# Performance work log

Hardware: AMD Instinct MI355X
Metric: run time of the kernel (lower is better)

## Reference

```python
import jax, jax.numpy as jnp
import numpy as np

N = 50000      # nodes
F_IN = 500     # in_channels
MID = 64       # mid_layer_channel
H = 2          # heads
OUT = 40       # out_channels
E = 800000     # edges per order
ORDER = 3
NEG_SLOPE = 0.2


def _gat(x, edge_index, W, a_src, a_dst, b, concat):
    # PyG-style GATConv (eval mode, dropout off), with self loops.
    n = x.shape[0]
    heads, ch = a_src.shape
    h = (x @ W).reshape(n, heads, ch)                    # [N,H,C]
    loop = jnp.arange(n)
    src = jnp.concatenate([edge_index[0], loop])
    dst = jnp.concatenate([edge_index[1], loop])
    al_s = jnp.sum(h * a_src, axis=-1)                   # [N,H]
    al_d = jnp.sum(h * a_dst, axis=-1)                   # [N,H]
    e = jax.nn.leaky_relu(al_s[src] + al_d[dst], NEG_SLOPE)   # [Etot,H]
    m = jax.ops.segment_max(e, dst, num_segments=n)      # softmax over incoming edges per dst
    ex = jnp.exp(e - m[dst])
    den = jax.ops.segment_sum(ex, dst, num_segments=n)
    alpha = ex / (den[dst] + 1e-16)
    out = jax.ops.segment_sum(alpha[:, :, None] * h[src], dst, num_segments=n)  # [N,H,C]
    if concat:
        return out.reshape(n, heads * ch) + b
    return out.mean(axis=1) + b


def _aggr(states, Wmix, wfin):
    # NOrderAggrConv (depth=2): mix order states with [order,order] weights + ELU,
    # then reduce to a single state with a learned [order] combination.
    h = jnp.stack(states, axis=1)                        # [N,order,C]
    h = jax.nn.elu(jnp.einsum('nkc,kj->njc', h, Wmix))
    return jnp.einsum('nkc,k->nc', h, wfin)


def setup_inputs():
    key = jax.random.key(0)
    ks = jax.random.split(key, 40)
    d = {}
    d['node_feature'] = jax.random.normal(ks[0], (N, F_IN), jnp.float32)
    for o in range(ORDER):
        d[f'adj{o}'] = jax.random.randint(ks[1 + o], (2, E), 0, N)
    i = 4
    s = 0.05
    layer_dims = [(F_IN, MID, H * MID), (MID * H, OUT, OUT)]
    for l, (fin, c, bdim) in enumerate(layer_dims):
        for o in range(ORDER):
            d[f'W_{l}_{o}'] = jax.random.normal(ks[i], (fin, H * c), jnp.float32) * s; i += 1
            d[f'as_{l}_{o}'] = jax.random.normal(ks[i], (H, c), jnp.float32) * s; i += 1
            d[f'ad_{l}_{o}'] = jax.random.normal(ks[i], (H, c), jnp.float32) * s; i += 1
            d[f'b_{l}_{o}'] = jnp.zeros((bdim,), jnp.float32)
    for l in range(2):
        d[f'agg{l}_W'] = jax.random.normal(ks[i], (ORDER, ORDER), jnp.float32) * 0.5; i += 1
        d[f'agg{l}_w'] = jnp.full((ORDER,), 1.0 / ORDER, jnp.float32)
    return d


def reference(node_feature, adj0, adj1, adj2,
              W_0_0, as_0_0, ad_0_0, b_0_0,
              W_0_1, as_0_1, ad_0_1, b_0_1,
              W_0_2, as_0_2, ad_0_2, b_0_2,
              W_1_0, as_1_0, ad_1_0, b_1_0,
              W_1_1, as_1_1, ad_1_1, b_1_1,
              W_1_2, as_1_2, ad_1_2, b_1_2,
              agg0_W, agg0_w, agg1_W, agg1_w):
    adjs = (adj0, adj1, adj2)
    p0 = ((W_0_0, as_0_0, ad_0_0, b_0_0),
          (W_0_1, as_0_1, ad_0_1, b_0_1),
          (W_0_2, as_0_2, ad_0_2, b_0_2))
    p1 = ((W_1_0, as_1_0, ad_1_0, b_1_0),
          (W_1_1, as_1_1, ad_1_1, b_1_1),
          (W_1_2, as_1_2, ad_1_2, b_1_2))
    aggs = ((agg0_W, agg0_w), (agg1_W, agg1_w))
    x = node_feature  # eval mode: dropout is identity
    for l, params in enumerate((p0, p1)):
        concat = (l == 0)
        states = [jax.nn.elu(_gat(x, adjs[o], *params[o], concat)) for o in range(ORDER)]
        x = _aggr(states, *aggs[l])
    return jax.nn.log_softmax(x, axis=1)
```

## Files before the change

kernel.cpp:

```cpp
#include <hip/hip_runtime.h>
#include <cstdint>
#include <cstddef>
#include <math.h>


typedef __attribute__((ext_vector_type(8))) short short8;
typedef __attribute__((ext_vector_type(4))) float f32x4;
typedef __attribute__((ext_vector_type(2))) float f32x2;

struct P3f { const float* p[3]; };
struct P3c { const int* p[3]; };

__device__ __forceinline__ float leakyf(float x) { return x > 0.f ? x : 0.2f * x; }
__device__ __forceinline__ float eluf(float x)   { return x > 0.f ? x : expm1f(x); }

__device__ __forceinline__ unsigned short bf16r(float x) {
  unsigned int u = __float_as_uint(x);
  u += 0x7fffu + ((u >> 16) & 1u);
  return (unsigned short)(u >> 16);
}
__device__ __forceinline__ float bflo(unsigned int u) { return __uint_as_float(u << 16); }
__device__ __forceinline__ float bfhi(unsigned int u) { return __uint_as_float(u & 0xffff0000u); }

__device__ __forceinline__ void bf8_fma2(uint4 q, float xx, f32x2* a) {
  f32x2 v0 = {bflo(q.x), bfhi(q.x)};
  f32x2 v1 = {bflo(q.y), bfhi(q.y)};
  f32x2 v2 = {bflo(q.z), bfhi(q.z)};
  f32x2 v3 = {bflo(q.w), bfhi(q.w)};
  a[0] += xx * v0;
  a[1] += xx * v1;
  a[2] += xx * v2;
  a[3] += xx * v3;
}

__global__ __launch_bounds__(256) void zero_int_kernel(int* p, int n) {
  int i = blockIdx.x * blockDim.x + threadIdx.x;
  if (i < n) p[i] = 0;
}

__global__ __launch_bounds__(256) void count3_kernel(P3c adj, int* __restrict__ cntb,
                                                     int E, int N) {
  int i = blockIdx.x * blockDim.x + threadIdx.x;
  int o = blockIdx.y;
  if (i < E) atomicAdd(&cntb[o * N + adj.p[o][E + i]], 1);
}

#define SCAN_T 256
#define SCAN_VPT 8
#define SCAN_TILE 2048

__global__ __launch_bounds__(SCAN_T) void scan1_kernel(const int* __restrict__ cntb,
    int* __restrict__ rowptrb, int* __restrict__ bsums, int N) {
  __shared__ int lds[SCAN_T];
  const int o = blockIdx.y;
  const int* cnt = cntb + o * N;
  int* rowptr = rowptrb + o * (N + 1);
  int t = threadIdx.x;
  int base = blockIdx.x * SCAN_TILE + t * SCAN_VPT;
  int v[SCAN_VPT];
  int s = 0;
#pragma unroll
  for (int i = 0; i < SCAN_VPT; ++i) {
    int idx = base + i;
    int x = (idx < N) ? cnt[idx] : 0;
    s += x;
    v[i] = s;
  }
  lds[t] = s;
  __syncthreads();
  for (int off = 1; off < SCAN_T; off <<= 1) {
    int add = (t >= off) ? lds[t - off] : 0;
    __syncthreads();
    lds[t] += add;
    __syncthreads();
  }
  int excl = (t > 0) ? lds[t - 1] : 0;
#pragma unroll
  for (int i = 0; i < SCAN_VPT; ++i) {
    int idx = base + i;
    if (idx < N) rowptr[idx + 1] = excl + v[i];
  }
  if (t == SCAN_T - 1) bsums[o * 64 + blockIdx.x] = lds[t];
}

__global__ void scan2_kernel(int* bsums, int nb, int* rowptrb, int N) {
  if (threadIdx.x == 0 && blockIdx.x == 0) {
    for (int o = 0; o < 3; ++o) {
      int run = 0;
      for (int i = 0; i < nb; ++i) {
        int x = bsums[o * 64 + i];
        bsums[o * 64 + i] = run;
        run += x;
      }
      rowptrb[o * (N + 1)] = 0;
    }
  }
}

__global__ __launch_bounds__(256) void scan3_kernel(int* __restrict__ rowptrb,
    const int* __restrict__ bsums, int N) {
  int idx = blockIdx.x * blockDim.x + threadIdx.x;
  int o = blockIdx.y;
  if (idx < N) rowptrb[o * (N + 1) + idx + 1] += bsums[o * 64 + idx / SCAN_TILE];
}

__global__ __launch_bounds__(256) void fill3_kernel(P3c adj,
    const int* __restrict__ rowptrb, int* __restrict__ curb,
    int* __restrict__ colvb, int* __restrict__ rowidb, int E, int N) {
  int i = blockIdx.x * blockDim.x + threadIdx.x;
  int o = blockIdx.y;
  if (i < E) {
    const int* a = adj.p[o];
    int d = a[E + i];
    int pos = atomicAdd(&curb[o * N + d], 1);
    size_t base = (size_t)o * E + rowptrb[o * (N + 1) + d] + pos;
    colvb[base] = a[i];
    rowidb[base] = d;
  }
}

__global__ __launch_bounds__(256) void edge_w_kernel(const int* __restrict__ colvb,
    const int* __restrict__ rowidb, const float2* __restrict__ alsB,
    const float2* __restrict__ aldB, float2* __restrict__ xeB, int E, int N) {
  int i = blockIdx.x * blockDim.x + threadIdx.x;
  int o = blockIdx.y;
  if (i >= E) return;
  size_t idx = (size_t)o * E + i;
  int s = colvb[idx];
  int d = rowidb[idx];
  float2 a = alsB[(size_t)o * N + s];
  float2 b = aldB[(size_t)o * N + d];
  xeB[idx] = make_float2(__expf(leakyf(a.x + b.x)), __expf(leakyf(a.y + b.y)));
}

__global__ __launch_bounds__(256) void conv_bt3_kernel(P3f W,
    unsigned short* __restrict__ BtB, int K, int NC, int Kpad) {
  int n = blockIdx.y;
  int o = blockIdx.z;
  int k = blockIdx.x * 256 + threadIdx.x;
  if (k >= Kpad) return;
  float v = (k < K) ? W.p[o][(size_t)k * NC + n] : 0.f;
  BtB[(size_t)o * NC * Kpad + (size_t)n * Kpad + k] = bf16r(v);
}

#define GBM 128
#define LDSTRIDE 40

template<int NT, bool ABF16>
__global__ __launch_bounds__(256) void mfma_gemm_kernel(
    const void* __restrict__ Av, const unsigned short* __restrict__ BtB,
    P3f asp, P3f adp, unsigned short* __restrict__ CbB,
    float2* __restrict__ alsB, float2* __restrict__ aldB, int M, int K) {
  constexpr int NC = NT * 16;
  constexpr int CH = NT * 8;
  __shared__ unsigned short As[GBM * LDSTRIDE];
  __shared__ unsigned short Bs[NC * LDSTRIDE];
  const int t = threadIdx.x;
  const int o = blockIdx.y;
  const int wave = t >> 6, lane = t & 63;
  const int quad = lane >> 4, l16 = lane & 15;
  const int m0 = blockIdx.x * GBM;
  const int Kpad = (K + 31) & ~31;
  const unsigned short* Bt = BtB + (size_t)o * NC * Kpad;
  unsigned short* Cb = CbB + (size_t)o * M * NC;
  float2* al_s = alsB + (size_t)o * M;
  float2* al_d = aldB + (size_t)o * M;
  const float* a_src = asp.p[o];
  const float* a_dst = adp.p[o];

  f32x4 acc[2][NT];
#pragma unroll
  for (int i = 0; i < 2; ++i)
#pragma unroll
    for (int j = 0; j < NT; ++j) acc[i][j] = (f32x4){0.f, 0.f, 0.f, 0.f};

  const int arow = t >> 1;
  const int akoff = (t & 1) * 16;
  const int gm = m0 + arow;
  const unsigned short* browp = Bt + (size_t)arow * Kpad;

  for (int k0 = 0; k0 < Kpad; k0 += 32) {
    if (k0) __syncthreads();
    const int kb = k0 + akoff;
    if constexpr (ABF16) {
      const unsigned short* arowp = (const unsigned short*)Av + (size_t)gm * K;
      uint4 q0 = {0, 0, 0, 0}, q1 = {0, 0, 0, 0};
      if (gm < M) {
        const uint4* p = (const uint4*)(arowp + kb);
        q0 = p[0]; q1 = p[1];
      }
      short8* dst = (short8*)&As[arow * LDSTRIDE + akoff];
      union { uint4 q; short8 s; } c0, c1;
      c0.q = q0; c1.q = q1;
      dst[0] = c0.s;
      dst[1] = c1.s;
    } else {
      const float* arowp = (const float*)Av + (size_t)gm * K;
      float v[16];
      if (gm < M && kb + 16 <= K) {
        const float4* p = (const float4*)(arowp + kb);
#pragma unroll
        for (int i = 0; i < 4; ++i) {
          float4 q = p[i];
          v[4 * i] = q.x; v[4 * i + 1] = q.y; v[4 * i + 2] = q.z; v[4 * i + 3] = q.w;
        }
      } else {
#pragma unroll
        for (int i = 0; i < 16; ++i)
          v[i] = (gm < M && kb + i < K) ? arowp[kb + i] : 0.f;
      }
      union { unsigned short u[16]; short8 s[2]; } pk;
#pragma unroll
      for (int i = 0; i < 16; ++i) pk.u[i] = bf16r(v[i]);
      short8* dst = (short8*)&As[arow * LDSTRIDE + akoff];
      dst[0] = pk.s[0];
      dst[1] = pk.s[1];
    }
    if (arow < NC) {
      const uint4* p = (const uint4*)(browp + k0 + akoff);
      uint4 q0 = p[0], q1 = p[1];
      short8* dst = (short8*)&Bs[arow * LDSTRIDE + akoff];
      union { uint4 q; short8 s; } c0, c1;
      c0.q = q0; c1.q = q1;
      dst[0] = c0.s;
      dst[1] = c1.s;
    }
    __syncthreads();
    short8 af[2];
#pragma unroll
    for (int rt = 0; rt < 2; ++rt)
      af[rt] = *(const short8*)&As[(wave * 32 + rt * 16 + l16) * LDSTRIDE + quad * 8];
    short8 bfv[NT];
#pragma unroll
    for (int ct = 0; ct < NT; ++ct)
      bfv[ct] = *(const short8*)&Bs[(ct * 16 + l16) * LDSTRIDE + quad * 8];
#pragma unroll
    for (int rt = 0; rt < 2; ++rt)
#pragma unroll
      for (int ct = 0; ct < NT; ++ct)
        acc[rt][ct] = __builtin_amdgcn_mfma_f32_16x16x32_bf16(af[rt], bfv[ct],
                                                              acc[rt][ct], 0, 0, 0);
  }
  float asv[NT], adv[NT];
#pragma unroll
  for (int ct = 0; ct < NT; ++ct) {
    int col = ct * 16 + l16;
    asv[ct] = a_src[col];
    adv[ct] = a_dst[col];
  }
#pragma unroll
  for (int rt = 0; rt < 2; ++rt) {
    int gr0 = m0 + wave * 32 + rt * 16 + quad * 4;
#pragma unroll
    for (int r = 0; r < 4; ++r) {
      int gr = gr0 + r;
      float ps0 = 0.f, ps1 = 0.f, pd0 = 0.f, pd1 = 0.f;
#pragma unroll
      for (int ct = 0; ct < NT; ++ct) {
        int col = ct * 16 + l16;
        float v = acc[rt][ct][r];
        if (gr < M) Cb[(size_t)gr * NC + col] = bf16r(v);
        if (col < CH) { ps0 += v * asv[ct]; pd0 += v * adv[ct]; }
        else          { ps1 += v * asv[ct]; pd1 += v * adv[ct]; }
      }
#pragma unroll
      for (int off = 1; off < 16; off <<= 1) {
        ps0 += __shfl_xor(ps0, off, 64);
        ps1 += __shfl_xor(ps1, off, 64);
        pd0 += __shfl_xor(pd0, off, 64);
        pd1 += __shfl_xor(pd1, off, 64);
      }
      if (l16 == 0 && gr < M) {
        al_s[gr] = make_float2(ps0, ps1);
        al_d[gr] = make_float2(pd0, pd1);
      }
    }
  }
}

template<int C, int CONCAT>
__global__ __launch_bounds__(256) void gat_aggr5_kernel(
    const unsigned short* __restrict__ hB, const float2* __restrict__ alsB,
    const float2* __restrict__ aldB, const int* __restrict__ rowptrB,
    const int* __restrict__ colvB, const float2* __restrict__ xeB,
    P3f biasp, unsigned short* __restrict__ outB, int N, int E) {
  constexpr int HC = 2 * C;
  constexpr int FL = HC / 8;
  constexpr int ES = 64 / FL;
  constexpr int HB = C / 8;
  constexpr int OW = CONCAT ? HC : C;
  const int o = blockIdx.y;
  const unsigned short* h = hB + (size_t)o * N * HC;
  const float2* al_s = alsB + (size_t)o * N;
  const float2* al_d = aldB + (size_t)o * N;
  const int* rowptr = rowptrB + o * (N + 1);
  const float* bias = biasp.p[o];
  unsigned short* out = outB + (size_t)o * N * OW;

  int w = (blockIdx.x * blockDim.x + threadIdx.x) >> 6;
  int lane = threadIdx.x & 63;
  if (w >= N) return;
  const int eslot = lane / FL;
  const int f4 = lane - eslot * FL;
  const bool glane = lane < ES * FL;
  const float2 ad = al_d[w];
  const float2 asf = al_s[w];
  const int beg = rowptr[w], end = rowptr[w + 1];
  const int deg = end - beg;
  const int* cp = colvB + (size_t)o * E + beg;
  const float2* xp = xeB + (size_t)o * E + beg;

  const float xs0 = __expf(leakyf(asf.x + ad.x));
  const float xs1 = __expf(leakyf(asf.y + ad.y));

  f32x2 acc[4] = {}, acc2[4] = {};
  float dp0 = 0.f, dp1 = 0.f;

  auto gstep = [&](int j, f32x2* a) {
    if (glane && j < deg) {
      int sj = cp[j];
      float2 x = xp[j];
      uint4 q = ((const uint4*)(h + (size_t)sj * HC))[f4];
      if (f4 == 0) { dp0 += x.x; dp1 += x.y; }
      bf8_fma2(q, (f4 < HB) ? x.x : x.y, a);
    }
  };

  for (int jj = 0; jj < deg; jj += 2 * ES) {
    gstep(jj + eslot, acc);
    gstep(jj + ES + eslot, acc2);
  }

#pragma unroll
  for (int off = 1; off < 64; off <<= 1) {
    dp0 += __shfl_xor(dp0, off, 64);
    dp1 += __shfl_xor(dp1, off, 64);
  }
  float den0 = dp0 + xs0, den1 = dp1 + xs1;

  if (eslot == 0) {
    uint4 q = ((const uint4*)(h + (size_t)w * HC))[f4];
    bf8_fma2(q, (f4 < HB) ? xs0 : xs1, acc);
  }
#pragma unroll
  for (int i = 0; i < 4; ++i) acc[i] += acc2[i];

  auto fold = [&](int off, int lim) {
#pragma unroll
    for (int i = 0; i < 4; ++i) {
      float t0 = __shfl(acc[i][0], lane + off, 64);
      float t1 = __shfl(acc[i][1], lane + off, 64);
      if (lane < lim) { acc[i][0] += t0; acc[i][1] += t1; }
    }
  };
  if (ES == 4) {
    fold(2 * FL, 2 * FL);
    fold(FL, FL);
  } else {
    fold(3 * FL, 3 * FL);
    fold(FL, FL);
    fold(2 * FL, FL);
  }

  float inv0 = 1.f / (den0 + 1e-16f), inv1 = 1.f / (den1 + 1e-16f);
  if (CONCAT) {
    if (lane < FL) {
      float xx = (f4 < HB) ? inv0 : inv1;
      const float* bp = bias + f4 * 8;
      unsigned int pk[4];
#pragma unroll
      for (int i = 0; i < 4; ++i) {
        unsigned short lo = bf16r(eluf(acc[i][0] * xx + bp[2 * i]));
        unsigned short hi = bf16r(eluf(acc[i][1] * xx + bp[2 * i + 1]));
        pk[i] = (unsigned int)lo | ((unsigned int)hi << 16);
      }
      ((uint4*)(out + (size_t)w * OW + f4 * 8))[0] = make_uint4(pk[0], pk[1], pk[2], pk[3]);
    }
  } else {
    float p[8];
#pragma unroll
    for (int i = 0; i < 4; ++i) {
      p[2 * i]     = __shfl(acc[i][0], lane + HB, 64);
      p[2 * i + 1] = __shfl(acc[i][1], lane + HB, 64);
    }
    if (lane < HB) {
      const float* bp = bias + f4 * 8;
      unsigned int pk[4];
#pragma unroll
      for (int i = 0; i < 4; ++i) {
        float v0 = 0.5f * (acc[i][0] * inv0 + p[2 * i] * inv1) + bp[2 * i];
        float v1 = 0.5f * (acc[i][1] * inv0 + p[2 * i + 1] * inv1) + bp[2 * i + 1];
        pk[i] = (unsigned int)bf16r(eluf(v0)) | ((unsigned int)bf16r(eluf(v1)) << 16);
      }
      ((uint4*)(out + (size_t)w * OW + f4 * 8))[0] = make_uint4(pk[0], pk[1], pk[2], pk[3]);
    }
  }
}

template<int BF16OUT>
__global__ __launch_bounds__(256) void mixb_kernel(const unsigned short* __restrict__ sb,
    const float* __restrict__ Wm, const float* __restrict__ wf,
    void* __restrict__ out, int perU) {
  int i = blockIdx.x * blockDim.x + threadIdx.x;
  if (i >= perU) return;
  const unsigned int* sp = (const unsigned int*)sb;
  unsigned int u0 = sp[i];
  unsigned int u1 = sp[perU + i];
  unsigned int u2 = sp[2 * perU + i];
  float a0 = bflo(u0), a1 = bfhi(u0);
  float b0 = bflo(u1), b1 = bfhi(u1);
  float c0 = bflo(u2), c1 = bfhi(u2);
  float r0 = 0.f, r1 = 0.f;
#pragma unroll
  for (int j = 0; j < 3; ++j) {
    float w0 = Wm[j], w1 = Wm[3 + j], w2 = Wm[6 + j], wj = wf[j];
    r0 += wj * eluf(a0 * w0 + b0 * w1 + c0 * w2);
    r1 += wj * eluf(a1 * w0 + b1 * w1 + c1 * w2);
  }
  if (BF16OUT) {
    ((unsigned int*)out)[i] = (unsigned int)bf16r(r0) | ((unsigned int)bf16r(r1) << 16);
  } else {
    ((float2*)out)[i] = make_float2(r0, r1);
  }
}

__global__ __launch_bounds__(256) void log_softmax_kernel(const float* __restrict__ x,
    float* __restrict__ out, int N, int C) {
  int w = (blockIdx.x * blockDim.x + threadIdx.x) >> 6;
  int lane = threadIdx.x & 63;
  if (w >= N) return;
  float v = (lane < C) ? x[(size_t)w * C + lane] : -INFINITY;
  float mx = v;
#pragma unroll
  for (int off = 1; off < 64; off <<= 1) mx = fmaxf(mx, __shfl_xor(mx, off, 64));
  float ex = (lane < C) ? expf(v - mx) : 0.f;
  float s = ex;
#pragma unroll
  for (int off = 1; off < 64; off <<= 1) s += __shfl_xor(s, off, 64);
  if (lane < C) out[(size_t)w * C + lane] = v - mx - logf(s);
}

extern "C" void kernel_launch(void* const* d_in, const int* in_sizes, int n_in,
                              void* d_out, int out_size, void* d_ws, size_t ws_size,
                              hipStream_t stream) {
  const int F_IN = 500;
  const int N = in_sizes[0] / F_IN;
  const int E = in_sizes[1] / 2;
  const int HC0 = 128;
  const int HC1 = 80;
  const int C1 = 40;
  const int K0pad = 512, K1pad = 128;

  const float* x0 = (const float*)d_in[0];
  P3c adj;
  adj.p[0] = (const int*)d_in[1];
  adj.p[1] = (const int*)d_in[2];
  adj.p[2] = (const int*)d_in[3];
  P3f W0p, as0p, ad0p, b0p, W1p, as1p, ad1p, b1p;
  for (int o = 0; o < 3; ++o) {
    W0p.p[o]  = (const float*)d_in[4 + 4 * o + 0];
    as0p.p[o] = (const float*)d_in[4 + 4 * o + 1];
    ad0p.p[o] = (const float*)d_in[4 + 4 * o + 2];
    b0p.p[o]  = (const float*)d_in[4 + 4 * o + 3];
    W1p.p[o]  = (const float*)d_in[16 + 4 * o + 0];
    as1p.p[o] = (const float*)d_in[16 + 4 * o + 1];
    ad1p.p[o] = (const float*)d_in[16 + 4 * o + 2];
    b1p.p[o]  = (const float*)d_in[16 + 4 * o + 3];
  }
  const float* agg0W = (const float*)d_in[28];
  const float* agg0w = (const float*)d_in[29];
  const float* agg1W = (const float*)d_in[30];
  const float* agg1w = (const float*)d_in[31];

  char* ws = (char*)d_ws;
  size_t off = 0;
  auto alloc = [&](size_t bytes) -> void* {
    off = (off + 255) & ~(size_t)255;
    void* p = ws + off;
    off += bytes;
    return p;
  };
  int* rowptrb = (int*)alloc((size_t)3 * (N + 1) * 4);
  int* colvb   = (int*)alloc((size_t)3 * E * 4);
  int* rowidb  = (int*)alloc((size_t)3 * E * 4);
  int* cntcur  = (int*)alloc((size_t)6 * N * 4);
  int* bsums   = (int*)alloc(3 * 64 * 4);
  unsigned short* hB  = (unsigned short*)alloc((size_t)3 * N * HC0 * 2);
  unsigned short* stB = (unsigned short*)alloc((size_t)3 * N * HC0 * 2);
  float* x2 = (float*)alloc((size_t)N * C1 * 4);
  float2* alsB = (float2*)alloc((size_t)3 * N * 8);
  float2* aldB = (float2*)alloc((size_t)3 * N * 8);
  float2* xeB  = (float2*)alloc((size_t)3 * E * 8);
  unsigned short* Bt0B = (unsigned short*)alloc((size_t)3 * HC0 * K0pad * 2);
  unsigned short* Bt1B = (unsigned short*)alloc((size_t)3 * HC1 * K1pad * 2);
  (void)ws_size;

  const int TB = 256;
  const int nbE = (E + TB - 1) / TB;
  const int nbN = (N + TB - 1) / TB;
  const int scanBlocks = (N + SCAN_TILE - 1) / SCAN_TILE;
  const int waveBlocks = (int)(((size_t)N * 64 + TB - 1) / TB);
  const int gemmBlocks = (N + GBM - 1) / GBM;

  conv_bt3_kernel<<<dim3((K0pad + 255) / 256, HC0, 3), TB, 0, stream>>>(W0p, Bt0B, F_IN, HC0, K0pad);
  conv_bt3_kernel<<<dim3((K1pad + 255) / 256, HC1, 3), TB, 0, stream>>>(W1p, Bt1B, HC0, HC1, K1pad);

  zero_int_kernel<<<(6 * N + TB - 1) / TB, TB, 0, stream>>>(cntcur, 6 * N);
  count3_kernel<<<dim3(nbE, 3), TB, 0, stream>>>(adj, cntcur, E, N);
  scan1_kernel<<<dim3(scanBlocks, 3), SCAN_T, 0, stream>>>(cntcur, rowptrb, bsums, N);
  scan2_kernel<<<1, 64, 0, stream>>>(bsums, scanBlocks, rowptrb, N);
  scan3_kernel<<<dim3(nbN, 3), TB, 0, stream>>>(rowptrb, bsums, N);
  fill3_kernel<<<dim3(nbE, 3), TB, 0, stream>>>(adj, rowptrb, cntcur + 3 * N, colvb, rowidb, E, N);

  mfma_gemm_kernel<8, false><<<dim3(gemmBlocks, 3), TB, 0, stream>>>(
      x0, Bt0B, as0p, ad0p, hB, alsB, aldB, N, F_IN);
  edge_w_kernel<<<dim3(nbE, 3), TB, 0, stream>>>(colvb, rowidb, alsB, aldB, xeB, E, N);
  gat_aggr5_kernel<64, 1><<<dim3(waveBlocks, 3), TB, 0, stream>>>(
      hB, alsB, aldB, rowptrb, colvb, xeB, b0p, stB, N, E);
  mixb_kernel<1><<<((N * HC0 / 2) + TB - 1) / TB, TB, 0, stream>>>(
      stB, agg0W, agg0w, stB, N * HC0 / 2);

  mfma_gemm_kernel<5, true><<<dim3(gemmBlocks, 3), TB, 0, stream>>>(
      stB, Bt1B, as1p, ad1p, hB, alsB, aldB, N, HC0);
  edge_w_kernel<<<dim3(nbE, 3), TB, 0, stream>>>(colvb, rowidb, alsB, aldB, xeB, E, N);
  gat_aggr5_kernel<40, 0><<<dim3(waveBlocks, 3), TB, 0, stream>>>(
      hB, alsB, aldB, rowptrb, colvb, xeB, b1p, stB, N, E);
  mixb_kernel<0><<<((N * C1 / 2) + TB - 1) / TB, TB, 0, stream>>>(
      stB, agg1W, agg1w, x2, N * C1 / 2);

  log_softmax_kernel<<<waveBlocks, TB, 0, stream>>>(x2, (float*)d_out, N, C1);
}
```

Baseline: 922.3 us.

## Pack edge source and weights into 16-byte records, unroll aggregation gathers

Removes the rowidb array. Edge weights are now computed per destination node, looping over its CSR row, and written as a packed uint4 record holding the source index and both head weights. The aggregation kernel reads one record per edge instead of two separate arrays, and is unrolled to four edges per step so more gathers are in flight. The cost is a larger record stream (16 bytes versus 12 per edge) and a per-node loop in the edge kernel with imbalanced, serial, poorly coalesced work.

After: 1.019 ms. +10.5%, slower.

```diff
diff --git a/kernel.cpp b/kernel.cpp
--- a/kernel.cpp
+++ b/kernel.cpp
@@ -106,31 +106,35 @@
 
 __global__ __launch_bounds__(256) void fill3_kernel(P3c adj,
     const int* __restrict__ rowptrb, int* __restrict__ curb,
-    int* __restrict__ colvb, int* __restrict__ rowidb, int E, int N) {
+    int* __restrict__ colvb, int E, int N) {
   int i = blockIdx.x * blockDim.x + threadIdx.x;
   int o = blockIdx.y;
   if (i < E) {
     const int* a = adj.p[o];
     int d = a[E + i];
     int pos = atomicAdd(&curb[o * N + d], 1);
-    size_t base = (size_t)o * E + rowptrb[o * (N + 1) + d] + pos;
-    colvb[base] = a[i];
-    rowidb[base] = d;
-  }
-}
-
-__global__ __launch_bounds__(256) void edge_w_kernel(const int* __restrict__ colvb,
-    const int* __restrict__ rowidb, const float2* __restrict__ alsB,
-    const float2* __restrict__ aldB, float2* __restrict__ xeB, int E, int N) {
-  int i = blockIdx.x * blockDim.x + threadIdx.x;
+    colvb[(size_t)o * E + rowptrb[o * (N + 1) + d] + pos] = a[i];
+  }
+}
+
+__global__ __launch_bounds__(256) void edge_rec_kernel(const int* __restrict__ colvb,
+    const int* __restrict__ rowptrb, const float2* __restrict__ alsB,
+    const float2* __restrict__ aldB, uint4* __restrict__ recB, int E, int N) {
+  int n = blockIdx.x * blockDim.x + threadIdx.x;
   int o = blockIdx.y;
-  if (i >= E) return;
-  size_t idx = (size_t)o * E + i;
-  int s = colvb[idx];
-  int d = rowidb[idx];
-  float2 a = alsB[(size_t)o * N + s];
-  float2 b = aldB[(size_t)o * N + d];
-  xeB[idx] = make_float2(__expf(leakyf(a.x + b.x)), __expf(leakyf(a.y + b.y)));
+  if (n >= N) return;
+  const float2 ad = aldB[(size_t)o * N + n];
+  const float2* als = alsB + (size_t)o * N;
+  const int* colv = colvb + (size_t)o * E;
+  uint4* rec = recB + (size_t)o * E;
+  int beg = rowptrb[o * (N + 1) + n], end = rowptrb[o * (N + 1) + n + 1];
+  for (int j = beg; j < end; ++j) {
+    int s = colv[j];
+    float2 a = als[s];
+    float x0 = __expf(leakyf(a.x + ad.x));
+    float x1 = __expf(leakyf(a.y + ad.y));
+    rec[j] = make_uint4((unsigned int)s, __float_as_uint(x0), __float_as_uint(x1), 0u);
+  }
 }
 
 __global__ __launch_bounds__(256) void conv_bt3_kernel(P3f W,
@@ -279,11 +283,11 @@
 }
 
 template<int C, int CONCAT>
-__global__ __launch_bounds__(256) void gat_aggr5_kernel(
+__global__ __launch_bounds__(256) void gat_aggr6_kernel(
     const unsigned short* __restrict__ hB, const float2* __restrict__ alsB,
     const float2* __restrict__ aldB, const int* __restrict__ rowptrB,
-    const int* __restrict__ colvB, const float2* __restrict__ xeB,
-    P3f biasp, unsigned short* __restrict__ outB, int N, int E) {
+    const uint4* __restrict__ recB, P3f biasp, unsigned short* __restrict__ outB,
+    int N, int E) {
   constexpr int HC = 2 * C;
   constexpr int FL = HC / 8;
   constexpr int ES = 64 / FL;
@@ -307,8 +311,7 @@
   const float2 asf = al_s[w];
   const int beg = rowptr[w], end = rowptr[w + 1];
   const int deg = end - beg;
-  const int* cp = colvB + (size_t)o * E + beg;
-  const float2* xp = xeB + (size_t)o * E + beg;
+  const uint4* rp = recB + (size_t)o * E + beg;
 
   const float xs0 = __expf(leakyf(asf.x + ad.x));
   const float xs1 = __expf(leakyf(asf.y + ad.y));
@@ -316,19 +319,41 @@
   f32x2 acc[4] = {}, acc2[4] = {};
   float dp0 = 0.f, dp1 = 0.f;
 
-  auto gstep = [&](int j, f32x2* a) {
-    if (glane && j < deg) {
-      int sj = cp[j];
-      float2 x = xp[j];
-      uint4 q = ((const uint4*)(h + (size_t)sj * HC))[f4];
-      if (f4 == 0) { dp0 += x.x; dp1 += x.y; }
-      bf8_fma2(q, (f4 < HB) ? x.x : x.y, a);
-    }
-  };
-
-  for (int jj = 0; jj < deg; jj += 2 * ES) {
-    gstep(jj + eslot, acc);
-    gstep(jj + ES + eslot, acc2);
+  for (int jj = 0; jj < deg; jj += 4 * ES) {
+    int j0 = jj + eslot, j1 = jj + ES + eslot, j2 = jj + 2 * ES + eslot,
+        j3 = jj + 3 * ES + eslot;
+    bool v0 = glane && j0 < deg, v1 = glane && j1 < deg,
+         v2 = glane && j2 < deg, v3 = glane && j3 < deg;
+    uint4 r0, r1, r2, r3;
+    if (v0) r0 = rp[j0];
+    if (v1) r1 = rp[j1];
+    if (v2) r2 = rp[j2];
+    if (v3) r3 = rp[j3];
+    uint4 q0, q1, q2, q3;
+    if (v0) q0 = ((const uint4*)(h + (size_t)r0.x * HC))[f4];
+    if (v1) q1 = ((const uint4*)(h + (size_t)r1.x * HC))[f4];
+    if (v2) q2 = ((const uint4*)(h + (size_t)r2.x * HC))[f4];
+    if (v3) q3 = ((const uint4*)(h + (size_t)r3.x * HC))[f4];
+    if (v0) {
+      float x0 = __uint_as_float(r0.y), x1 = __uint_as_float(r0.z);
+      if (f4 == 0) { dp0 += x0; dp1 += x1; }
+      bf8_fma2(q0, (f4 < HB) ? x0 : x1, acc);
+    }
+    if (v1) {
+      float x0 = __uint_as_float(r1.y), x1 = __uint_as_float(r1.z);
+      if (f4 == 0) { dp0 += x0; dp1 += x1; }
+      bf8_fma2(q1, (f4 < HB) ? x0 : x1, acc2);
+    }
+    if (v2) {
+      float x0 = __uint_as_float(r2.y), x1 = __uint_as_float(r2.z);
+      if (f4 == 0) { dp0 += x0; dp1 += x1; }
+      bf8_fma2(q2, (f4 < HB) ? x0 : x1, acc);
+    }
+    if (v3) {
+      float x0 = __uint_as_float(r3.y), x1 = __uint_as_float(r3.z);
+      if (f4 == 0) { dp0 += x0; dp1 += x1; }
+      bf8_fma2(q3, (f4 < HB) ? x0 : x1, acc2);
+    }
   }
 
 #pragma unroll
@@ -482,7 +507,6 @@
   };
   int* rowptrb = (int*)alloc((size_t)3 * (N + 1) * 4);
   int* colvb   = (int*)alloc((size_t)3 * E * 4);
-  int* rowidb  = (int*)alloc((size_t)3 * E * 4);
   int* cntcur  = (int*)alloc((size_t)6 * N * 4);
   int* bsums   = (int*)alloc(3 * 64 * 4);
   unsigned short* hB  = (unsigned short*)alloc((size_t)3 * N * HC0 * 2);
@@ -490,7 +514,7 @@
   float* x2 = (float*)alloc((size_t)N * C1 * 4);
   float2* alsB = (float2*)alloc((size_t)3 * N * 8);
   float2* aldB = (float2*)alloc((size_t)3 * N * 8);
-  float2* xeB  = (float2*)alloc((size_t)3 * E * 8);
+  uint4* recB  = (uint4*)alloc((size_t)3 * E * 16);
   unsigned short* Bt0B = (unsigned short*)alloc((size_t)3 * HC0 * K0pad * 2);
   unsigned short* Bt1B = (unsigned short*)alloc((size_t)3 * HC1 * K1pad * 2);
   (void)ws_size;
@@ -510,21 +534,21 @@
   scan1_kernel<<<dim3(scanBlocks, 3), SCAN_T, 0, stream>>>(cntcur, rowptrb, bsums, N);
   scan2_kernel<<<1, 64, 0, stream>>>(bsums, scanBlocks, rowptrb, N);
   scan3_kernel<<<dim3(nbN, 3), TB, 0, stream>>>(rowptrb, bsums, N);
-  fill3_kernel<<<dim3(nbE, 3), TB, 0, stream>>>(adj, rowptrb, cntcur + 3 * N, colvb, rowidb, E, N);
+  fill3_kernel<<<dim3(nbE, 3), TB, 0, stream>>>(adj, rowptrb, cntcur + 3 * N, colvb, E, N);
 
   mfma_gemm_kernel<8, false><<<dim3(gemmBlocks, 3), TB, 0, stream>>>(
       x0, Bt0B, as0p, ad0p, hB, alsB, aldB, N, F_IN);
-  edge_w_kernel<<<dim3(nbE, 3), TB, 0, stream>>>(colvb, rowidb, alsB, aldB, xeB, E, N);
-  gat_aggr5_kernel<64, 1><<<dim3(waveBlocks, 3), TB, 0, stream>>>(
-      hB, alsB, aldB, rowptrb, colvb, xeB, b0p, stB, N, E);
+  edge_rec_kernel<<<dim3(nbN, 3), TB, 0, stream>>>(colvb, rowptrb, alsB, aldB, recB, E, N);
+  gat_aggr6_kernel<64, 1><<<dim3(waveBlocks, 3), TB, 0, stream>>>(
+      hB, alsB, aldB, rowptrb, recB, b0p, stB, N, E);
   mixb_kernel<1><<<((N * HC0 / 2) + TB - 1) / TB, TB, 0, stream>>>(
       stB, agg0W, agg0w, stB, N * HC0 / 2);
 
   mfma_gemm_kernel<5, true><<<dim3(gemmBlocks, 3), TB, 0, stream>>>(
       stB, Bt1B, as1p, ad1p, hB, alsB, aldB, N, HC0);
-  edge_w_kernel<<<dim3(nbE, 3), TB, 0, stream>>>(colvb, rowidb, alsB, aldB, xeB, E, N);
-  gat_aggr5_kernel<40, 0><<<dim3(waveBlocks, 3), TB, 0, stream>>>(
-      hB, alsB, aldB, rowptrb, colvb, xeB, b1p, stB, N, E);
+  edge_rec_kernel<<<dim3(nbN, 3), TB, 0, stream>>>(colvb, rowptrb, alsB, aldB, recB, E, N);
+  gat_aggr6_kernel<40, 0><<<dim3(waveBlocks, 3), TB, 0, stream>>>(
+      hB, alsB, aldB, rowptrb, recB, b1p, stB, N, E);
   mixb_kernel<0><<<((N * C1 / 2) + TB - 1) / TB, TB, 0, stream>>>(
       stB, agg1W, agg1w, x2, N * C1 / 2);
 
```
